# Optimization experiments

Hardware: AMD Instinct MI355X
Metric: run time of the kernel (lower is better)

Reference implementation:

```python
import jax, jax.numpy as jnp
import numpy as np

HEADS = 7
DIM_HEAD = 64
SCALE = DIM_HEAD ** -0.5


def setup_inputs() -> dict:
    key = jax.random.key(0)
    ks = jax.random.split(key, 6)
    b, n, dim = 8, 1024, 448
    inner = HEADS * DIM_HEAD  # 448
    x = jax.random.normal(ks[0], (b, n, dim), dtype=jnp.float32)
    w_qv = jax.random.normal(ks[1], (dim, 2 * inner), dtype=jnp.float32) * 0.02
    ext_k = jax.random.normal(ks[2], (HEADS, n, DIM_HEAD), dtype=jnp.float32)
    ext_bias = jax.random.normal(ks[3], (HEADS, n, n), dtype=jnp.float32)
    w_out = jax.random.normal(ks[4], (inner, dim), dtype=jnp.float32) * 0.02
    b_out = jnp.zeros((dim,), dtype=jnp.float32)
    return {"x": x, "w_qv": w_qv, "ext_k": ext_k, "ext_bias": ext_bias,
            "w_out": w_out, "b_out": b_out}


def reference(x, w_qv, ext_k, ext_bias, w_out, b_out):
    b, n, dim = x.shape
    qv = x @ w_qv                                   # [b, n, 2*inner]
    q, v = jnp.split(qv, 2, axis=-1)
    # b n (h d) -> b h n d
    q = q.reshape(b, n, HEADS, DIM_HEAD).transpose(0, 2, 1, 3)
    v = v.reshape(b, n, HEADS, DIM_HEAD).transpose(0, 2, 1, 3)
    # scores vs external learned key, additive bias applied BEFORE scale
    dots = (jnp.einsum('bhnd,hmd->bhnm', q, ext_k) + ext_bias[None]) * SCALE
    attn = jax.nn.softmax(dots, axis=-1)
    out = jnp.einsum('bhnm,bhmd->bhnd', attn, v)
    out = out.transpose(0, 2, 1, 3).reshape(b, n, HEADS * DIM_HEAD)
    return out @ w_out + b_out  # dropout is identity in eval mode
```

## Files before the change

### kernel.cpp

```cpp
#include <hip/hip_runtime.h>
#include <hip/hip_bf16.h>
#include <hip/hip_fp16.h>

#define BATCH 8
#define NSEQ 1024
#define DIMM 448
#define NHEAD 7
#define HDIM 64
#define MROWS (BATCH*NSEQ)
#define KDIM 448
#define SCALE_F 0.125f
#define PSTR 66048

typedef short short8 __attribute__((ext_vector_type(8)));
typedef float floatx16 __attribute__((ext_vector_type(16)));

#define MFMA32(a,b,c) __builtin_amdgcn_mfma_f32_32x32x16_bf16(a,b,c,0,0,0)

__device__ __forceinline__ unsigned short f2bf(float f){
    __hip_bfloat16 h = __float2bfloat16(f);
    return *reinterpret_cast<unsigned short*>(&h);
}
__device__ __forceinline__ float bf2f(unsigned short u){
    __hip_bfloat16 h; *reinterpret_cast<unsigned short*>(&h) = u;
    return __bfloat162float(h);
}
__device__ __forceinline__ float h2f(unsigned short u){
    __half h; *reinterpret_cast<unsigned short*>(&h) = u;
    return __half2float(h);
}
__device__ __forceinline__ unsigned short f2h(float f){
    __half h = __float2half(f);
    return *reinterpret_cast<unsigned short*>(&h);
}

__global__ __launch_bounds__(256)
void prep_min(const float* __restrict__ x, const float* __restrict__ wqv,
              unsigned short* __restrict__ xh, unsigned short* __restrict__ wqvTh)
{
    const int bx = blockIdx.x, tid = threadIdx.x;
    if (bx < 3584) {
        int i = bx*256 + tid;
        float4 v = ((const float4*)x)[i];
        ((ushort4*)xh)[i] = make_ushort4(f2bf(v.x), f2bf(v.y), f2bf(v.z), f2bf(v.w));
    } else {
        int lid = (bx-3584)*4 + (tid>>6);
        int kc = lid % 56, ng = lid / 56;
        int n = ng*64 + (tid&63);
        unsigned short h[8];
#pragma unroll
        for (int j = 0; j < 8; ++j) h[j] = f2bf(wqv[(size_t)(kc*8+j)*896 + n]);
        size_t o = (size_t)n*KDIM + kc*8;
        *(ushort4*)(wqvTh + o)     = make_ushort4(h[0],h[1],h[2],h[3]);
        *(ushort4*)(wqvTh + o + 4) = make_ushort4(h[4],h[5],h[6],h[7]);
    }
}

__global__ __launch_bounds__(256, 2)
void gemm1_fused(const unsigned short* __restrict__ Ah, const unsigned short* __restrict__ Bh,
                 const float* __restrict__ ek, const float* __restrict__ eb,
                 const float* __restrict__ wout,
                 unsigned short* __restrict__ qd, unsigned short* __restrict__ vTd,
                 unsigned short* __restrict__ ekh, unsigned short* __restrict__ bp,
                 unsigned short* __restrict__ woTh, unsigned short* __restrict__ woTl)
{
    __shared__ float T[2][64][33];
    const int bx = blockIdx.x, tid = threadIdx.x;

    if (bx < 448) {
        const int w = tid >> 6, lane = tid & 63;
        const int lq = lane & 31, lh = lane >> 5;
        const int xb = bx & 31, y = bx >> 5;
        const int m0 = (xb*4 + w) * 64;
        const int n0 = y * 64;
        const unsigned short* aB = Ah + (size_t)(m0 + lq)*KDIM + lh*8;
        const unsigned short* bB = Bh + (size_t)(n0 + lq)*KDIM + lh*8;

        floatx16 acc[2][2] = {};
        short8 aR[2][2][2], bR[2][2][2];
#define LD1(kt, par) {                                                        \
    _Pragma("unroll") for (int fm = 0; fm < 2; ++fm)                          \
    _Pragma("unroll") for (int c = 0; c < 2; ++c) {                           \
        aR[par][fm][c] = *(const short8*)(aB + (size_t)fm*32*KDIM + (kt)*32 + c*16); \
        bR[par][fm][c] = *(const short8*)(bB + (size_t)fm*32*KDIM + (kt)*32 + c*16); } }

        LD1(0, 0)
#pragma unroll
        for (int kt = 0; kt < 14; ++kt) {
            const int par = kt & 1;
            if (kt < 13) LD1(kt+1, par^1)
#pragma unroll
            for (int c = 0; c < 2; ++c)
#pragma unroll
                for (int fm = 0; fm < 2; ++fm)
#pragma unroll
                    for (int fn = 0; fn < 2; ++fn)
                        acc[fm][fn] = MFMA32(aR[par][fm][c], bR[par][fn][c], acc[fm][fn]);
        }
#undef LD1

        if (y < NHEAD) {
#pragma unroll
            for (int fm = 0; fm < 2; ++fm)
#pragma unroll
                for (int fn = 0; fn < 2; ++fn) {
                    const int d = fn*32 + lq;
#pragma unroll
                    for (int r = 0; r < 16; ++r) {
                        const int gm = m0 + fm*32 + (r&3) + 8*(r>>2) + 4*lh;
                        const int b = gm >> 10, ns = gm & 1023;
                        qd[((size_t)((b*NHEAD + y)*NSEQ + ns))*HDIM + d] = f2bf(acc[fm][fn][r]);
                    }
                }
        } else {
            const int head = y - NHEAD;
#pragma unroll
            for (int fm = 0; fm < 2; ++fm) {
                const int gm0 = m0 + fm*32;
                const int b = gm0 >> 10, mm = (gm0 & 1023) >> 5;
                unsigned short* base = vTd + (size_t)(b*NHEAD + head)*PSTR + (size_t)mm*2048;
#pragma unroll
                for (int fn = 0; fn < 2; ++fn)
#pragma unroll
                    for (int rq = 0; rq < 4; ++rq) {
                        const int u = (rq>>1)*2 + fn;
                        const int lanep = (rq&1)*32 + lq;
                        *(ushort4*)(base + u*512 + lanep*8 + 4*lh) = make_ushort4(
                            f2bf(acc[fm][fn][rq*4+0]), f2bf(acc[fm][fn][rq*4+1]),
                            f2bf(acc[fm][fn][rq*4+2]), f2bf(acc[fm][fn][rq*4+3]));
                    }
            }
        }
    } else if (bx < 2240) {
        const int sub = tid >> 7, st = tid & 127;
        const int lid = (bx-448)*2 + sub;
        const int mt = lid & 31, qt = (lid>>5) & 15, h = lid >> 9;
#pragma unroll
        for (int it = 0; it < 4; ++it) {
            int idx = it*128 + st;
            int row = idx >> 3, c4 = (idx & 7)*4;
            float4 v = *(const float4*)(eb + ((size_t)(h*NSEQ + qt*64 + row))*NSEQ + mt*32 + c4);
            T[sub][row][c4+0]=v.x; T[sub][row][c4+1]=v.y;
            T[sub][row][c4+2]=v.z; T[sub][row][c4+3]=v.w;
        }
        __syncthreads();
        const int g2 = st >> 6, lane = st & 63;
        const int lq = lane & 31, quad = lane >> 5;
        const int q = g2*32 + lq;
        unsigned short* dst = bp + (size_t)(h*16 + qt)*PSTR
                            + (size_t)(mt*4 + g2*2)*512 + lane*8;
#pragma unroll
        for (int jj = 0; jj < 2; ++jj) {
            unsigned short o[8];
#pragma unroll
            for (int t = 0; t < 8; ++t) {
                int m = (t&3) + 8*(t>>2) + 16*jj + 4*quad;
                o[t] = f2h(T[sub][q][m] * SCALE_F);
            }
            *(ushort4*)(dst + jj*512)     = make_ushort4(o[0],o[1],o[2],o[3]);
            *(ushort4*)(dst + jj*512 + 4) = make_ushort4(o[4],o[5],o[6],o[7]);
        }
    } else if (bx < 2688) {
        int i = (bx-2240)*256 + tid;
        const int h  = i >> 14, mm = (i >> 9) & 31, c = (i >> 7) & 3;
        const int ln = (i >> 1) & 63, jh = i & 1;
        const float* src = ek + ((size_t)(h*NSEQ) + mm*32 + (ln & 31))*HDIM
                              + c*16 + (ln >> 5)*8 + jh*4;
        float4 v = *(const float4*)src;
        unsigned short* dst = ekh + (size_t)h*PSTR + (size_t)(i & 16383)*4;
        *(ushort4*)dst = make_ushort4(f2bf(v.x), f2bf(v.y), f2bf(v.z), f2bf(v.w));
    } else {
        int lid = (bx-2688)*4 + (tid>>6);
        int kc = lid % 56, ng = lid / 56;
        int n = ng*64 + (tid&63);
        ushort4 h0={0,0,0,0}, h1={0,0,0,0}, l0={0,0,0,0}, l1={0,0,0,0};
        if (n < DIMM) {
            unsigned short h[8], l[8];
#pragma unroll
            for (int j = 0; j < 8; ++j) {
                float f = wout[(size_t)(kc*8+j)*DIMM + n];
                h[j] = f2bf(f); l[j] = f2bf(f - bf2f(h[j]));
            }
            h0 = make_ushort4(h[0],h[1],h[2],h[3]); h1 = make_ushort4(h[4],h[5],h[6],h[7]);
            l0 = make_ushort4(l[0],l[1],l[2],l[3]); l1 = make_ushort4(l[4],l[5],l[6],l[7]);
        }
        size_t o = (size_t)n*KDIM + kc*8;
        *(ushort4*)(woTh + o) = h0; *(ushort4*)(woTh + o + 4) = h1;
        *(ushort4*)(woTl + o) = l0; *(ushort4*)(woTl + o + 4) = l1;
    }
}

__global__ __launch_bounds__(256, 2)
void attn_half(const unsigned short* __restrict__ qh_g, const unsigned short* __restrict__ vTh,
               const unsigned short* __restrict__ ekh, const unsigned short* __restrict__ bp,
               float4* __restrict__ opart, float2* __restrict__ lspart)
{
    const int tid = threadIdx.x;
    const int w = tid >> 6, lane = tid & 63;
    const int lq = lane & 31, lh = lane >> 5;

    const int orig = blockIdx.x;
    const int wg = (orig & 7)*56 + (orig >> 3);
    const int half = wg & 1, bq = (wg >> 1) & 1, qt = (wg >> 2) & 15, head = wg >> 6;
    const int b = bq*4 + w;
    const int bh = b*NHEAD + head;
    const int mBeg = half*16;

    short8 qf[2][4];
#pragma unroll
    for (int g2 = 0; g2 < 2; ++g2)
#pragma unroll
        for (int c = 0; c < 4; ++c)
            qf[g2][c] = *(const short8*)(qh_g +
                ((size_t)(bh*NSEQ) + qt*64 + g2*32 + lq)*HDIM + c*16 + lh*8);

    const unsigned short* kB = ekh + (size_t)head*PSTR + lane*8;
    const unsigned short* vB = vTh + (size_t)bh*PSTR + lane*8;
    const unsigned short* bB = bp + (size_t)(head*16 + qt)*PSTR + lane*8;

    short8 kR[2][4], vR[2][4], bR[2][4];
#define PREF(J, par) { const int mm = ((J) < mBeg+16) ? (J) : mBeg;            \
    _Pragma("unroll") for (int c = 0; c < 4; ++c)                              \
        kR[par][c] = *(const short8*)(kB + (size_t)mm*2048 + c*512);           \
    _Pragma("unroll") for (int u = 0; u < 4; ++u)                              \
        vR[par][u] = *(const short8*)(vB + (size_t)mm*2048 + u*512);           \
    _Pragma("unroll") for (int u = 0; u < 4; ++u)                              \
        bR[par][u] = *(const short8*)(bB + (size_t)mm*2048 + u*512); }

    floatx16 O[2][2] = {};
    float ls[2] = {0.f, 0.f};

#define SEC(J, par, nxt) {                                                     \
    PREF((J)+1, nxt)                                                           \
    _Pragma("unroll") for (int g2 = 0; g2 < 2; ++g2) {                         \
        floatx16 S = {};                                                       \
        _Pragma("unroll") for (int c = 0; c < 4; ++c)                          \
            S = MFMA32(kR[par][c], qf[g2][c], S);                              \
        float pv[16];                                                          \
        _Pragma("unroll") for (int i = 0; i < 16; ++i) {                       \
            float bs = h2f((unsigned short)bR[par][g2*2 + (i>>3)][i&7]);       \
            pv[i] = __expf(fmaf(S[i], SCALE_F, bs));                           \
            ls[g2] += pv[i];                                                   \
        }                                                                      \
        unsigned wpk[8];                                                       \
        _Pragma("unroll") for (int u = 0; u < 8; ++u)                          \
            wpk[u] = (unsigned)f2bf(pv[2*u]) | ((unsigned)f2bf(pv[2*u+1]) << 16); \
        asm("v_permlane32_swap_b32 %0, %1" : "+v"(wpk[0]), "+v"(wpk[2]));      \
        asm("v_permlane32_swap_b32 %0, %1" : "+v"(wpk[1]), "+v"(wpk[3]));      \
        asm("v_permlane32_swap_b32 %0, %1" : "+v"(wpk[4]), "+v"(wpk[6]));      \
        asm("v_permlane32_swap_b32 %0, %1" : "+v"(wpk[5]), "+v"(wpk[7]));      \
        union U8 { unsigned u[4]; short8 s; };                                 \
        U8 pa0, pa1;                                                           \
        pa0.u[0]=wpk[0]; pa0.u[1]=wpk[1]; pa0.u[2]=wpk[2]; pa0.u[3]=wpk[3];    \
        pa1.u[0]=wpk[4]; pa1.u[1]=wpk[5]; pa1.u[2]=wpk[6]; pa1.u[3]=wpk[7];    \
        O[g2][0] = MFMA32(pa0.s, vR[par][0], O[g2][0]);                        \
        O[g2][1] = MFMA32(pa0.s, vR[par][1], O[g2][1]);                        \
        O[g2][0] = MFMA32(pa1.s, vR[par][2], O[g2][0]);                        \
        O[g2][1] = MFMA32(pa1.s, vR[par][3], O[g2][1]);                        \
    } }

    PREF(mBeg, 0)
    for (int jj = 0; jj < 8; ++jj) {
        SEC(mBeg+2*jj,   0, 1)
        SEC(mBeg+2*jj+1, 1, 0)
    }
#undef SEC
#undef PREF

    const int tile = (head*16 + qt)*8 + b;
    const int wid = tile*2 + half;
    float4* ob = opart + (size_t)wid*1024;
#pragma unroll
    for (int g2 = 0; g2 < 2; ++g2)
#pragma unroll
        for (int fn = 0; fn < 2; ++fn)
#pragma unroll
            for (int r4 = 0; r4 < 4; ++r4)
                ob[((g2*2+fn)*4 + r4)*64 + lane] = make_float4(
                    O[g2][fn][r4*4+0], O[g2][fn][r4*4+1],
                    O[g2][fn][r4*4+2], O[g2][fn][r4*4+3]);
    lspart[(size_t)wid*64 + lane] = make_float2(ls[0], ls[1]);
}

__global__ __launch_bounds__(256, 2)
void attn_combine(const float4* __restrict__ opart, const float2* __restrict__ lspart,
                  unsigned short* __restrict__ aoh, unsigned short* __restrict__ aol)
{
    __shared__ float linv[4][2][32];
    const int tid = threadIdx.x;
    const int w = tid >> 6, lane = tid & 63;
    const int lq = lane & 31, lh = lane >> 5;

    const int t = blockIdx.x*4 + w;
    const int b = t & 7, qt = (t >> 3) & 15, head = t >> 7;

    const float2 la = lspart[(size_t)(t*2)*64 + lane];
    const float2 lb = lspart[(size_t)(t*2+1)*64 + lane];
    float ls0 = la.x + lb.x, ls1 = la.y + lb.y;
    float lt0 = ls0 + __shfl_xor(ls0, 32);
    float lt1 = ls1 + __shfl_xor(ls1, 32);
    if (lh == 0) { linv[w][0][lq] = 1.f/lt0; linv[w][1][lq] = 1.f/lt1; }

    const float4* oa = opart + (size_t)(t*2)*1024;
    const float4* ob = opart + (size_t)(t*2+1)*1024;
#pragma unroll
    for (int g2 = 0; g2 < 2; ++g2)
#pragma unroll
        for (int fn = 0; fn < 2; ++fn)
#pragma unroll
            for (int r4 = 0; r4 < 4; ++r4) {
                const int ch = ((g2*2+fn)*4 + r4)*64 + lane;
                float4 va = oa[ch], vb = ob[ch];
                float s[4] = {va.x+vb.x, va.y+vb.y, va.z+vb.z, va.w+vb.w};
#pragma unroll
                for (int j = 0; j < 4; ++j) {
                    const int qr = j + 8*r4 + 4*lh;
                    const float inv = linv[w][g2][qr];
                    const size_t o = ((size_t)(b*NSEQ) + qt*64 + g2*32 + qr)*DIMM
                                   + head*HDIM + fn*32 + lq;
                    float v = s[j]*inv;
                    unsigned short h0 = f2bf(v);
                    aoh[o] = h0;  aol[o] = f2bf(v - bf2f(h0));
                }
            }
}

__global__ __launch_bounds__(128, 2)
void gemm2_grp(const unsigned short* __restrict__ Ah, const unsigned short* __restrict__ Al,
               const unsigned short* __restrict__ Bh, const unsigned short* __restrict__ Bl,
               const float* __restrict__ bias, float* __restrict__ out)
{
    const int tid = threadIdx.x;
    const int w = tid >> 6, lane = tid & 63;
    const int lq = lane & 31, lh = lane >> 5;
    const int m0 = (blockIdx.x*2 + w) * 64;
    const int n0 = blockIdx.y * 64;
    const unsigned short* aBh = Ah + (size_t)(m0 + lq)*KDIM + lh*8;
    const unsigned short* aBl = Al + (size_t)(m0 + lq)*KDIM + lh*8;
    const unsigned short* bBh = Bh + (size_t)(n0 + lq)*KDIM + lh*8;
    const unsigned short* bBl = Bl + (size_t)(n0 + lq)*KDIM + lh*8;

    floatx16 acc[2][2] = {};
    short8 aH[2][2][2], aL[2][2][2], bH[2][2][2], bL[2][2][2];
#define LD2(kt, par) {                                                        \
    _Pragma("unroll") for (int fm = 0; fm < 2; ++fm)                          \
    _Pragma("unroll") for (int c = 0; c < 2; ++c) {                           \
        const size_t off = (size_t)fm*32*KDIM + (kt)*32 + c*16;               \
        aH[par][fm][c] = *(const short8*)(aBh + off);                         \
        aL[par][fm][c] = *(const short8*)(aBl + off);                         \
        bH[par][fm][c] = *(const short8*)(bBh + off);                         \
        bL[par][fm][c] = *(const short8*)(bBl + off); } }

    LD2(0, 0)
#pragma unroll
    for (int kt = 0; kt < 14; ++kt) {
        const int par = kt & 1;
        if (kt < 13) LD2(kt+1, par^1)
#pragma unroll
        for (int c = 0; c < 2; ++c)
#pragma unroll
            for (int fm = 0; fm < 2; ++fm)
#pragma unroll
                for (int fn = 0; fn < 2; ++fn) {
                    acc[fm][fn] = MFMA32(aH[par][fm][c], bH[par][fn][c], acc[fm][fn]);
                    acc[fm][fn] = MFMA32(aL[par][fm][c], bH[par][fn][c], acc[fm][fn]);
                    acc[fm][fn] = MFMA32(aH[par][fm][c], bL[par][fn][c], acc[fm][fn]);
                }
    }
#undef LD2

#pragma unroll
    for (int fm = 0; fm < 2; ++fm)
#pragma unroll
        for (int fn = 0; fn < 2; ++fn) {
            const int gn = n0 + fn*32 + lq;
            const float bv = bias[gn];
#pragma unroll
            for (int r = 0; r < 16; ++r) {
                const int gm = m0 + fm*32 + (r&3) + 8*(r>>2) + 4*lh;
                out[(size_t)gm*DIMM + gn] = acc[fm][fn][r] + bv;
            }
        }
}

extern "C" void kernel_launch(void* const* d_in, const int* in_sizes, int n_in,
                              void* d_out, int out_size, void* d_ws, size_t ws_size,
                              hipStream_t stream)
{
    const float* x    = (const float*)d_in[0];
    const float* wqv  = (const float*)d_in[1];
    const float* ek   = (const float*)d_in[2];
    const float* eb   = (const float*)d_in[3];
    const float* wout = (const float*)d_in[4];
    const float* bout = (const float*)d_in[5];
    float* out = (float*)d_out;

    const size_t MK = (size_t)MROWS*KDIM;
    unsigned short* p = (unsigned short*)d_ws;
    unsigned short* xh    = p;  p += MK;
    unsigned short* wqvTh = p;  p += (size_t)896*KDIM;
    unsigned short* woTh  = p;  p += (size_t)512*KDIM;
    unsigned short* woTl  = p;  p += (size_t)512*KDIM;
    unsigned short* ekh   = p;  p += (size_t)NHEAD*PSTR;
    unsigned short* qh    = p;  p += MK;
    unsigned short* vTh   = p;  p += (size_t)BATCH*NHEAD*PSTR;
    unsigned short* bp    = p;  p += (size_t)NHEAD*16*PSTR;
    unsigned short* aoh   = p;  p += MK;
    unsigned short* aol   = p;  p += MK;
    float4* opart  = (float4*)p;
    p += (size_t)1792*1024*8;
    float2* lspart = (float2*)p;
    p += (size_t)1792*64*4;

    prep_min<<<3780, 256, 0, stream>>>(x, wqv, xh, wqvTh);
    gemm1_fused<<<2800, 256, 0, stream>>>(xh, wqvTh, ek, eb, wout,
                                          qh, vTh, ekh, bp, woTh, woTl);
    attn_half<<<448, 256, 0, stream>>>(qh, vTh, ekh, bp, opart, lspart);
    attn_combine<<<224, 256, 0, stream>>>(opart, lspart, aoh, aol);
    gemm2_grp<<<dim3(64, 7), 128, 0, stream>>>(aoh, aol, woTh, woTl, bout, out);
}
```

Measured before the change: 192.7 us.

## Fuse split-KV combine into attention kernel via atomic last-arriver reduction

Removes the separate attn_combine launch. Each attention wave writes its partial output and row sums, then bumps a per-tile atomic counter, and the second-arriving half reads its sibling's partials and produces the normalized bf16 hi/lo output directly. The flag buffer is zeroed inside the prep kernel. This saves one kernel launch and one full read of the partials from the slower half's registers, at the cost of threadfences and atomics, and the counter relies on ordering through memory fences.

```diff
diff --git a/kernel.cpp b/kernel.cpp
--- a/kernel.cpp
+++ b/kernel.cpp
@@ -36,14 +36,15 @@
 
 __global__ __launch_bounds__(256)
 void prep_min(const float* __restrict__ x, const float* __restrict__ wqv,
-              unsigned short* __restrict__ xh, unsigned short* __restrict__ wqvTh)
+              unsigned short* __restrict__ xh, unsigned short* __restrict__ wqvTh,
+              unsigned* __restrict__ flags)
 {
     const int bx = blockIdx.x, tid = threadIdx.x;
     if (bx < 3584) {
         int i = bx*256 + tid;
         float4 v = ((const float4*)x)[i];
         ((ushort4*)xh)[i] = make_ushort4(f2bf(v.x), f2bf(v.y), f2bf(v.z), f2bf(v.w));
-    } else {
+    } else if (bx < 3780) {
         int lid = (bx-3584)*4 + (tid>>6);
         int kc = lid % 56, ng = lid / 56;
         int n = ng*64 + (tid&63);
@@ -53,6 +54,8 @@
         size_t o = (size_t)n*KDIM + kc*8;
         *(ushort4*)(wqvTh + o)     = make_ushort4(h[0],h[1],h[2],h[3]);
         *(ushort4*)(wqvTh + o + 4) = make_ushort4(h[4],h[5],h[6],h[7]);
+    } else {
+        for (int i = tid; i < 896; i += 256) flags[i] = 0u;
     }
 }
 
@@ -191,10 +194,13 @@
 }
 
 __global__ __launch_bounds__(256, 2)
-void attn_half(const unsigned short* __restrict__ qh_g, const unsigned short* __restrict__ vTh,
-               const unsigned short* __restrict__ ekh, const unsigned short* __restrict__ bp,
-               float4* __restrict__ opart, float2* __restrict__ lspart)
+void attn_skc(const unsigned short* __restrict__ qh_g, const unsigned short* __restrict__ vTh,
+              const unsigned short* __restrict__ ekh, const unsigned short* __restrict__ bp,
+              float4* __restrict__ opart, float2* __restrict__ lspart,
+              unsigned* __restrict__ flags,
+              unsigned short* __restrict__ aoh, unsigned short* __restrict__ aol)
 {
+    __shared__ float linv[4][2][32];
     const int tid = threadIdx.x;
     const int w = tid >> 6, lane = tid & 63;
     const int lq = lane & 31, lh = lane >> 5;
@@ -280,49 +286,43 @@
                     O[g2][fn][r4*4+0], O[g2][fn][r4*4+1],
                     O[g2][fn][r4*4+2], O[g2][fn][r4*4+3]);
     lspart[(size_t)wid*64 + lane] = make_float2(ls[0], ls[1]);
-}
-
-__global__ __launch_bounds__(256, 2)
-void attn_combine(const float4* __restrict__ opart, const float2* __restrict__ lspart,
-                  unsigned short* __restrict__ aoh, unsigned short* __restrict__ aol)
-{
-    __shared__ float linv[4][2][32];
-    const int tid = threadIdx.x;
-    const int w = tid >> 6, lane = tid & 63;
-    const int lq = lane & 31, lh = lane >> 5;
-
-    const int t = blockIdx.x*4 + w;
-    const int b = t & 7, qt = (t >> 3) & 15, head = t >> 7;
-
-    const float2 la = lspart[(size_t)(t*2)*64 + lane];
-    const float2 lb = lspart[(size_t)(t*2+1)*64 + lane];
-    float ls0 = la.x + lb.x, ls1 = la.y + lb.y;
-    float lt0 = ls0 + __shfl_xor(ls0, 32);
-    float lt1 = ls1 + __shfl_xor(ls1, 32);
-    if (lh == 0) { linv[w][0][lq] = 1.f/lt0; linv[w][1][lq] = 1.f/lt1; }
-
-    const float4* oa = opart + (size_t)(t*2)*1024;
-    const float4* ob = opart + (size_t)(t*2+1)*1024;
-#pragma unroll
-    for (int g2 = 0; g2 < 2; ++g2)
-#pragma unroll
-        for (int fn = 0; fn < 2; ++fn)
-#pragma unroll
-            for (int r4 = 0; r4 < 4; ++r4) {
-                const int ch = ((g2*2+fn)*4 + r4)*64 + lane;
-                float4 va = oa[ch], vb = ob[ch];
-                float s[4] = {va.x+vb.x, va.y+vb.y, va.z+vb.z, va.w+vb.w};
-#pragma unroll
-                for (int j = 0; j < 4; ++j) {
-                    const int qr = j + 8*r4 + 4*lh;
-                    const float inv = linv[w][g2][qr];
-                    const size_t o = ((size_t)(b*NSEQ) + qt*64 + g2*32 + qr)*DIMM
-                                   + head*HDIM + fn*32 + lq;
-                    float v = s[j]*inv;
-                    unsigned short h0 = f2bf(v);
-                    aoh[o] = h0;  aol[o] = f2bf(v - bf2f(h0));
+
+    __threadfence();
+    unsigned old = 0;
+    if (lane == 0) old = atomicAdd(&flags[tile], 1u);
+    old = __shfl(old, 0);
+    if (old == 1) {
+        __threadfence();
+        const int sib = tile*2 + (1 - half);
+        const float2 lb = lspart[(size_t)sib*64 + lane];
+        float lt0p = ls[0] + lb.x, lt1p = ls[1] + lb.y;
+        float lt0 = lt0p + __shfl_xor(lt0p, 32);
+        float lt1 = lt1p + __shfl_xor(lt1p, 32);
+        if (lh == 0) { linv[w][0][lq] = 1.f/lt0; linv[w][1][lq] = 1.f/lt1; }
+
+        const float4* oa = opart + (size_t)sib*1024;
+#pragma unroll
+        for (int g2 = 0; g2 < 2; ++g2)
+#pragma unroll
+            for (int fn = 0; fn < 2; ++fn)
+#pragma unroll
+                for (int r4 = 0; r4 < 4; ++r4) {
+                    const int ch = ((g2*2+fn)*4 + r4)*64 + lane;
+                    float4 vb = oa[ch];
+                    float s[4] = {O[g2][fn][r4*4+0]+vb.x, O[g2][fn][r4*4+1]+vb.y,
+                                  O[g2][fn][r4*4+2]+vb.z, O[g2][fn][r4*4+3]+vb.w};
+#pragma unroll
+                    for (int j = 0; j < 4; ++j) {
+                        const int qr = j + 8*r4 + 4*lh;
+                        const float inv = linv[w][g2][qr];
+                        const size_t o = ((size_t)(b*NSEQ) + qt*64 + g2*32 + qr)*DIMM
+                                       + head*HDIM + fn*32 + lq;
+                        float v = s[j]*inv;
+                        unsigned short h0 = f2bf(v);
+                        aoh[o] = h0;  aol[o] = f2bf(v - bf2f(h0));
+                    }
                 }
-            }
+    }
 }
 
 __global__ __launch_bounds__(128, 2)
@@ -411,11 +411,12 @@
     p += (size_t)1792*1024*8;
     float2* lspart = (float2*)p;
     p += (size_t)1792*64*4;
-
-    prep_min<<<3780, 256, 0, stream>>>(x, wqv, xh, wqvTh);
+    unsigned* flags = (unsigned*)p;
+    p += (size_t)896*2;
+
+    prep_min<<<3781, 256, 0, stream>>>(x, wqv, xh, wqvTh, flags);
     gemm1_fused<<<2800, 256, 0, stream>>>(xh, wqvTh, ek, eb, wout,
                                           qh, vTh, ekh, bp, woTh, woTl);
-    attn_half<<<448, 256, 0, stream>>>(qh, vTh, ekh, bp, opart, lspart);
-    attn_combine<<<224, 256, 0, stream>>>(opart, lspart, aoh, aol);
+    attn_skc<<<448, 256, 0, stream>>>(qh, vTh, ekh, bp, opart, lspart, flags, aoh, aol);
     gemm2_grp<<<dim3(64, 7), 128, 0, stream>>>(aoh, aol, woTh, woTl, bout, out);
 }
```

Result: slower. 278.3 us (+44.4%).
